# Optimization experiments

Measured on AMD Instinct MI355X. Metric: run time of the kernel, lower is better.

Reference implementation:

```python
import jax, jax.numpy as jnp
import numpy as np

B, C, H, W = 2048, 512, 4, 4
T, D, NH, HD, FF, NL = 16, 512, 8, 64, 1024, 4
EPS = 1e-5
SCALE = float(1.0 / np.sqrt(HD))


def _make_adj(h, w):
    # torch_geometric.utils.grid(h, w): 3x3 neighborhood incl. self-loop;
    # GCNConv sym-normalizes: A_hat = D^-1/2 A D^-1/2
    n = h * w
    A = np.zeros((n, n), np.float32)
    for r in range(h):
        for c in range(w):
            for dr in (-1, 0, 1):
                for dc in (-1, 0, 1):
                    rr, cc = r + dr, c + dc
                    if 0 <= rr < h and 0 <= cc < w:
                        A[r * w + c, rr * w + cc] = 1.0
    dinv = 1.0 / np.sqrt(A.sum(1))
    return (A * dinv[:, None] * dinv[None, :]).astype(np.float32)


def setup_inputs():
    key = jax.random.key(0)
    ks = iter(jax.random.split(key, 64))
    def w(*s):
        return jax.random.normal(next(ks), s, jnp.float32) * 0.02
    return dict(
        x=jax.random.normal(next(ks), (B, C, H, W), jnp.float32),
        emb_w=w(D, D), emb_b=jnp.zeros((D,), jnp.float32),
        emb_ln_g=jnp.ones((D,), jnp.float32), emb_ln_b=jnp.zeros((D,), jnp.float32),
        pos=w(1, T, D),
        attn_wq=w(NL, D, D), attn_wk=w(NL, D, D), attn_wv=w(NL, D, D),
        attn_bq=jnp.zeros((NL, D), jnp.float32), attn_bk=jnp.zeros((NL, D), jnp.float32),
        attn_bv=jnp.zeros((NL, D), jnp.float32),
        attn_wo=w(NL, D, D), attn_bo=jnp.zeros((NL, D), jnp.float32),
        ln1_g=jnp.ones((NL, D), jnp.float32), ln1_b=jnp.zeros((NL, D), jnp.float32),
        ff_w1=w(NL, D, FF), ff_b1=jnp.zeros((NL, FF), jnp.float32),
        ff_w2=w(NL, FF, D), ff_b2=jnp.zeros((NL, D), jnp.float32),
        ln2_g=jnp.ones((NL, D), jnp.float32), ln2_b=jnp.zeros((NL, D), jnp.float32),
        fc_w=w(D, D), fc_b=jnp.zeros((D,), jnp.float32),
        fc_ln_g=jnp.ones((D,), jnp.float32), fc_ln_b=jnp.zeros((D,), jnp.float32),
        gcn_w1=w(C, 2 * C), gcn_b1=jnp.zeros((2 * C,), jnp.float32),
        gcn_ln1_g=jnp.ones((2 * C,), jnp.float32), gcn_ln1_b=jnp.zeros((2 * C,), jnp.float32),
        gcn_w2=w(2 * C, C), gcn_b2=jnp.zeros((C,), jnp.float32),
        gcn_ln2_g=jnp.ones((C,), jnp.float32), gcn_ln2_b=jnp.zeros((C,), jnp.float32),
        fusion_w=w(C, 2 * C), fusion_b=jnp.zeros((C,), jnp.float32),
        adj=jnp.asarray(_make_adj(H, W)),
    )


def _ln(x, g, b):
    mu = x.mean(-1, keepdims=True)
    var = ((x - mu) ** 2).mean(-1, keepdims=True)
    return (x - mu) * jax.lax.rsqrt(var + EPS) * g + b


def reference(x, emb_w, emb_b, emb_ln_g, emb_ln_b, pos,
              attn_wq, attn_wk, attn_wv, attn_bq, attn_bk, attn_bv, attn_wo, attn_bo,
              ln1_g, ln1_b, ff_w1, ff_b1, ff_w2, ff_b2, ln2_g, ln2_b,
              fc_w, fc_b, fc_ln_g, fc_ln_b,
              gcn_w1, gcn_b1, gcn_ln1_g, gcn_ln1_b, gcn_w2, gcn_b2, gcn_ln2_g, gcn_ln2_b,
              fusion_w, fusion_b, adj):
    Bx = x.shape[0]
    # ---- transformer branch: tokens = 16 spatial positions, dim 512 ----
    h = x.reshape(Bx, C, T).transpose(0, 2, 1)                 # [B,T,D]
    h = _ln(h @ emb_w + emb_b, emb_ln_g, emb_ln_b) + pos
    for i in range(NL):  # post-norm TransformerEncoderLayer, ReLU, eval (no dropout)
        q = (h @ attn_wq[i] + attn_bq[i]).reshape(Bx, T, NH, HD).transpose(0, 2, 1, 3)
        k = (h @ attn_wk[i] + attn_bk[i]).reshape(Bx, T, NH, HD).transpose(0, 2, 1, 3)
        v = (h @ attn_wv[i] + attn_bv[i]).reshape(Bx, T, NH, HD).transpose(0, 2, 1, 3)
        a = jax.nn.softmax(jnp.einsum('bhqd,bhkd->bhqk', q, k) * SCALE, axis=-1)
        o = jnp.einsum('bhqk,bhkd->bhqd', a, v).transpose(0, 2, 1, 3).reshape(Bx, T, D)
        h = _ln(h + o @ attn_wo[i] + attn_bo[i], ln1_g[i], ln1_b[i])
        f = jax.nn.relu(h @ ff_w1[i] + ff_b1[i]) @ ff_w2[i] + ff_b2[i]
        h = _ln(h + f, ln2_g[i], ln2_b[i])
    h = _ln(h @ fc_w + fc_b, fc_ln_g, fc_ln_b)
    x1 = h.transpose(0, 2, 1).reshape(Bx, C, H, W)
    # ---- GCN branch: dense normalized adjacency over the 16-node grid ----
    xn = x.transpose(0, 2, 3, 1).reshape(Bx, T, C)             # [B,16,C]
    g = jnp.einsum('mn,bnd->bmd', adj, xn @ gcn_w1) + gcn_b1   # GCNConv1 (bias after aggr)
    g = jax.nn.elu(_ln(g, gcn_ln1_g, gcn_ln1_b))
    g = jnp.einsum('mn,bnd->bmd', adj, g @ gcn_w2) + gcn_b2    # GCNConv2
    g = jax.nn.elu(_ln(g, gcn_ln2_g, gcn_ln2_b))
    x2 = g.reshape(Bx, H, W, C).transpose(0, 3, 1, 2)
    # ---- fusion: 1x1 conv + InstanceNorm2d (no affine) + ELU ----
    xc = jnp.concatenate([x1, x2], axis=1)                     # [B,2C,H,W]
    y = jnp.einsum('oc,bchw->bohw', fusion_w, xc) + fusion_b[None, :, None, None]
    mu = y.mean((2, 3), keepdims=True)
    var = ((y - mu) ** 2).mean((2, 3), keepdims=True)
    y = (y - mu) * jax.lax.rsqrt(var + EPS)
    return jax.nn.elu(y)
```

## Files before the change

### kernel.cpp

```cpp
#include <hip/hip_runtime.h>


typedef _Float16 f16;
typedef f16 f16x8 __attribute__((ext_vector_type(8)));
typedef f16 f16x4 __attribute__((ext_vector_type(4)));
typedef float f32x4 __attribute__((ext_vector_type(4)));

__device__ inline float wred_sum(float s) {
#pragma unroll
  for (int m = 32; m; m >>= 1) s += __shfl_xor(s, m);
  return s;
}

struct WDesc {
  const float* src;
  f16* dst;
  int K, N, tiles_n, tile_base, mode;
};
struct WTable {
  WDesc d[32];
  int n;
};

__global__ void wconvert_kernel(WTable tab) {
  const int tile = blockIdx.x;
  int di = 0;
  while (di + 1 < tab.n && tab.d[di + 1].tile_base <= tile) ++di;
  const WDesc w = tab.d[di];
  const int t = tile - w.tile_base;
  const int tk = t / w.tiles_n, tn = t % w.tiles_n;
  const int tid = threadIdx.x;
  const int rr = tid >> 5, cc = tid & 31;
  __shared__ float tb[32][33];
  if (w.mode == 0) {
#pragma unroll
    for (int i = 0; i < 4; i++) {
      const int k = tk * 32 + i * 8 + rr, n = tn * 32 + cc;
      tb[i * 8 + rr][cc] = w.src[(size_t)k * w.N + n];
    }
    __syncthreads();
#pragma unroll
    for (int i = 0; i < 4; i++) {
      const int n = tn * 32 + i * 8 + rr, k = tk * 32 + cc;
      w.dst[(size_t)n * w.K + k] = (f16)tb[cc][i * 8 + rr];
    }
  } else {
#pragma unroll
    for (int i = 0; i < 4; i++) {
      const int k = tk * 32 + i * 8 + rr, n = tn * 32 + cc;
      w.dst[(size_t)k * w.N + n] = (f16)w.src[(size_t)k * w.N + n];
    }
  }
}

__global__ void biaspack_kernel(const float* __restrict__ bq,
                                const float* __restrict__ bk,
                                const float* __restrict__ bv,
                                float* __restrict__ bqkv) {
  const int i = blockIdx.x * 256 + threadIdx.x;
  if (i >= 4 * 1536) return;
  const int l = i / 1536, j = i % 1536;
  float v;
  if (j < 512)       v = bq[l * 512 + j];
  else if (j < 1024) v = bk[l * 512 + j - 512];
  else               v = bv[l * 512 + j - 1024];
  bqkv[i] = v;
}

__global__ void prep_kernel(const float* __restrict__ x, f16* __restrict__ X0) {
  const int b = blockIdx.x;
  for (int c = threadIdx.x; c < 512; c += 256) {
    const float* src = x + ((size_t)b * 512 + c) * 16;
    float vals[16];
#pragma unroll
    for (int i = 0; i < 4; i++) {
      const float4 v = ((const float4*)src)[i];
      vals[i * 4 + 0] = v.x; vals[i * 4 + 1] = v.y;
      vals[i * 4 + 2] = v.z; vals[i * 4 + 3] = v.w;
    }
#pragma unroll
    for (int t = 0; t < 16; t++)
      X0[((size_t)b * 16 + t) * 512 + c] = (f16)vals[t];
  }
}

template <int OUT, bool RELU, bool HASB>
__global__ __launch_bounds__(256) void gemm_kernel(
    const f16* __restrict__ A, const f16* __restrict__ Bt, void* __restrict__ C,
    const float* __restrict__ bias, int N, int K, int lda, int ldb) {
  __shared__ alignas(16) f16 sm[3][8192];
  const int tid = threadIdx.x;
  const int nb = N >> 7;
  const int cpx = gridDim.x >> 3;
  const int wg = (blockIdx.x & 7) * cpx + (blockIdx.x >> 3);
  const int bx = wg % nb;
  const int by = wg / nb;
  const int row0 = by << 7, col0 = bx << 7;
  const int lane = tid & 63;
  const int wave = tid >> 6;
  const int wm = (wave >> 1) << 6;
  const int wn = (wave & 1) << 6;
  const int srow = tid >> 2;
  const int schunk = (tid & 3) ^ ((tid >> 3) & 3);
  const f16* gA = A + (size_t)(row0 + srow) * lda + (schunk << 3);
  const f16* gB = Bt + (size_t)(col0 + srow) * ldb + (schunk << 3);
  const int wave_off = (tid & 0xC0) << 3;
  f32x4 acc[4][4] = {};
  const int rm = lane & 15;
  const int kg = lane >> 4;
  const int nt = K >> 5;

  auto STAGE = [&](int t, int bufi) {
    f16* lA = sm[bufi] + wave_off;
    f16* lB = sm[bufi] + 4096 + wave_off;
    const int kt = t << 5;
    __builtin_amdgcn_global_load_lds(
        (const __attribute__((address_space(1))) void*)(gA + kt),
        (__attribute__((address_space(3))) void*)lA, 16, 0, 0);
    __builtin_amdgcn_global_load_lds(
        (const __attribute__((address_space(1))) void*)(gA + (size_t)64 * lda + kt),
        (__attribute__((address_space(3))) void*)(lA + 2048), 16, 0, 0);
    __builtin_amdgcn_global_load_lds(
        (const __attribute__((address_space(1))) void*)(gB + kt),
        (__attribute__((address_space(3))) void*)lB, 16, 0, 0);
    __builtin_amdgcn_global_load_lds(
        (const __attribute__((address_space(1))) void*)(gB + (size_t)64 * ldb + kt),
        (__attribute__((address_space(3))) void*)(lB + 2048), 16, 0, 0);
  };

  STAGE(0, 0);
  STAGE(1, 1);
  asm volatile("s_waitcnt vmcnt(4)" ::: "memory");
  __builtin_amdgcn_s_barrier();

  for (int t = 0; t < nt; ++t) {
    const int cur = t % 3;
    if (t + 2 < nt) STAGE(t + 2, (t + 2) % 3);
    const f16* As = sm[cur];
    const f16* Bs = sm[cur] + 4096;
    f16x8 af[4], bf[4];
#pragma unroll
    for (int m = 0; m < 4; ++m) {
      const int r = wm + m * 16 + rm;
      af[m] = *(const f16x8*)(As + (r << 5) + ((kg ^ ((r >> 1) & 3)) << 3));
    }
#pragma unroll
    for (int n = 0; n < 4; ++n) {
      const int r = wn + n * 16 + rm;
      bf[n] = *(const f16x8*)(Bs + (r << 5) + ((kg ^ ((r >> 1) & 3)) << 3));
    }
#pragma unroll
    for (int m = 0; m < 4; ++m)
#pragma unroll
      for (int n = 0; n < 4; ++n)
        acc[m][n] =
            __builtin_amdgcn_mfma_f32_16x16x32_f16(af[m], bf[n], acc[m][n], 0, 0, 0);
    if (t + 2 < nt) {
      asm volatile("s_waitcnt vmcnt(4)" ::: "memory");
    } else {
      asm volatile("s_waitcnt vmcnt(0)" ::: "memory");
    }
    __builtin_amdgcn_s_barrier();
  }

  const int cn = lane & 15;
  const int rg = (lane >> 4) << 2;
  if (OUT == 3) {
    float* out = (float*)C;
#pragma unroll
    for (int m = 0; m < 4; ++m) {
      const int bidx = (row0 >> 4) + (wm >> 4) + m;
#pragma unroll
      for (int n = 0; n < 4; ++n) {
        const int col = col0 + wn + n * 16 + cn;
        const float v0 = acc[m][n][0], v1 = acc[m][n][1];
        const float v2 = acc[m][n][2], v3 = acc[m][n][3];
        float s = v0 + v1 + v2 + v3;
        s += __shfl_xor(s, 16);
        s += __shfl_xor(s, 32);
        const float mu = s * (1.f / 16.f);
        float q = (v0 - mu) * (v0 - mu) + (v1 - mu) * (v1 - mu) +
                  (v2 - mu) * (v2 - mu) + (v3 - mu) * (v3 - mu);
        q += __shfl_xor(q, 16);
        q += __shfl_xor(q, 32);
        const float rstd = rsqrtf(q * (1.f / 16.f) + 1e-5f);
        float4 z;
        z.x = (v0 - mu) * rstd; z.x = z.x > 0.f ? z.x : expm1f(z.x);
        z.y = (v1 - mu) * rstd; z.y = z.y > 0.f ? z.y : expm1f(z.y);
        z.z = (v2 - mu) * rstd; z.z = z.z > 0.f ? z.z : expm1f(z.z);
        z.w = (v3 - mu) * rstd; z.w = z.w > 0.f ? z.w : expm1f(z.w);
        *(float4*)(out + ((size_t)bidx * 512 + col) * 16 + rg) = z;
      }
    }
  } else {
#pragma unroll
    for (int m = 0; m < 4; ++m) {
#pragma unroll
      for (int n = 0; n < 4; ++n) {
        const int col = col0 + wn + n * 16 + cn;
        const float bv = HASB ? bias[col] : 0.0f;
#pragma unroll
        for (int r = 0; r < 4; ++r) {
          const int row = row0 + wm + m * 16 + rg + r;
          float v = acc[m][n][r] + bv;
          if (RELU) v = v > 0.f ? v : 0.f;
          ((f16*)C)[(size_t)row * N + col] = (f16)v;
        }
      }
    }
  }
}

template <bool RES, bool POS>
__global__ void ln_kernel(const f16* in, const f16* res, const float* g,
                          const float* b, const float* pos, f16* out) {
  const int row = (blockIdx.x << 2) + (threadIdx.x >> 6);
  const int lane = threadIdx.x & 63;
  const int c0 = lane << 3;
  float v[8];
  const f16x8 xi = *(const f16x8*)(in + (size_t)row * 512 + c0);
  if (RES) {
    const f16x8 ri = *(const f16x8*)(res + (size_t)row * 512 + c0);
#pragma unroll
    for (int j = 0; j < 8; j++) v[j] = (float)xi[j] + (float)ri[j];
  } else {
#pragma unroll
    for (int j = 0; j < 8; j++) v[j] = (float)xi[j];
  }
  float s = 0;
#pragma unroll
  for (int j = 0; j < 8; j++) s += v[j];
  s = wred_sum(s);
  const float mu = s * (1.f / 512.f);
  float q = 0;
#pragma unroll
  for (int j = 0; j < 8; j++) {
    const float d = v[j] - mu;
    q += d * d;
  }
  q = wred_sum(q);
  const float rstd = rsqrtf(q * (1.f / 512.f) + 1e-5f);
  const int t = row & 15;
  f16x8 o8;
#pragma unroll
  for (int j = 0; j < 8; j++) {
    float o = (v[j] - mu) * rstd * g[c0 + j] + b[c0 + j];
    if (POS) o += pos[t * 512 + c0 + j];
    o8[j] = (f16)o;
  }
  *(f16x8*)(out + (size_t)row * 512 + c0) = o8;
}

__global__ void lnpack_kernel(const f16* __restrict__ in, const f16* __restrict__ x2,
                              const float* __restrict__ g, const float* __restrict__ b,
                              f16* __restrict__ F) {
  const int row = (blockIdx.x << 2) + (threadIdx.x >> 6);
  const int lane = threadIdx.x & 63;
  const int c0 = lane << 3;
  const f16x8 xi = *(const f16x8*)(in + (size_t)row * 512 + c0);
  float v[8];
#pragma unroll
  for (int j = 0; j < 8; j++) v[j] = (float)xi[j];
  float s = 0;
#pragma unroll
  for (int j = 0; j < 8; j++) s += v[j];
  s = wred_sum(s);
  const float mu = s * (1.f / 512.f);
  float q = 0;
#pragma unroll
  for (int j = 0; j < 8; j++) {
    const float d = v[j] - mu;
    q += d * d;
  }
  q = wred_sum(q);
  const float rstd = rsqrtf(q * (1.f / 512.f) + 1e-5f);
  f16x8 o8;
#pragma unroll
  for (int j = 0; j < 8; j++)
    o8[j] = (f16)((v[j] - mu) * rstd * g[c0 + j] + b[c0 + j]);
  *(f16x8*)(F + (size_t)row * 1024 + c0) = o8;
  const f16x8 x2v = *(const f16x8*)(x2 + (size_t)row * 512 + c0);
  *(f16x8*)(F + (size_t)row * 1024 + 512 + c0) = x2v;
}

__global__ __launch_bounds__(256) void attn_kernel(const f16* __restrict__ qkv,
                                                   f16* __restrict__ o) {
  __shared__ f16 smem[4][3776];
  const int wid = threadIdx.x >> 6;
  const int lane = threadIdx.x & 63;
  const int bh = (blockIdx.x << 2) + wid;
  const int b = bh >> 3, h = bh & 7;
  f16* W = smem[wid];
  f16* Qw = W;
  f16* Kw = W + 1152;
  f16* Vw = W + 2304;
  f16* Pw = W + 3456;
  const size_t base = (size_t)b * 24576 + (size_t)h * 64;
#pragma unroll
  for (int i = 0; i < 6; i++) {
    const int c = i * 64 + lane;
    const int t = c / 24;
    const int rem = c - t * 24;
    const int mat = rem >> 3, ch = rem & 7;
    const f16x8 v = *(const f16x8*)(qkv + base + (size_t)t * 1536 + mat * 512 + ch * 8);
    *(f16x8*)(W + mat * 1152 + t * 72 + ch * 8) = v;
  }
  __syncthreads();
  const int rm = lane & 15, kg = lane >> 4;
  f32x4 s4 = {};
  {
    const f16x8 q0 = *(const f16x8*)(Qw + rm * 72 + kg * 8);
    const f16x8 q1 = *(const f16x8*)(Qw + rm * 72 + 32 + kg * 8);
    const f16x8 k0 = *(const f16x8*)(Kw + rm * 72 + kg * 8);
    const f16x8 k1 = *(const f16x8*)(Kw + rm * 72 + 32 + kg * 8);
    s4 = __builtin_amdgcn_mfma_f32_16x16x32_f16(q0, k0, s4, 0, 0, 0);
    s4 = __builtin_amdgcn_mfma_f32_16x16x32_f16(q1, k1, s4, 0, 0, 0);
  }
  float p[4];
#pragma unroll
  for (int r = 0; r < 4; r++) {
    const float sv = s4[r] * 0.125f;
    float m = sv;
    m = fmaxf(m, __shfl_xor(m, 1));
    m = fmaxf(m, __shfl_xor(m, 2));
    m = fmaxf(m, __shfl_xor(m, 4));
    m = fmaxf(m, __shfl_xor(m, 8));
    const float e = expf(sv - m);
    float s = e;
    s += __shfl_xor(s, 1);
    s += __shfl_xor(s, 2);
    s += __shfl_xor(s, 4);
    s += __shfl_xor(s, 8);
    p[r] = e / s;
  }
#pragma unroll
  for (int r = 0; r < 4; r++) Pw[(kg * 4 + r) * 20 + rm] = (f16)p[r];
  __syncthreads();
  const f16x4 pa = *(const f16x4*)(Pw + rm * 20 + kg * 4);
  f32x4 o4[4] = {};
#pragma unroll
  for (int dt = 0; dt < 4; dt++) {
    f16x4 vb;
#pragma unroll
    for (int kk = 0; kk < 4; kk++) vb[kk] = Vw[(kg * 4 + kk) * 72 + dt * 16 + rm];
    o4[dt] = __builtin_amdgcn_mfma_f32_16x16x16f16(pa, vb, o4[dt], 0, 0, 0);
  }
  f16* op = o + (size_t)b * 16 * 512 + (size_t)h * 64;
#pragma unroll
  for (int dt = 0; dt < 4; dt++)
#pragma unroll
    for (int r = 0; r < 4; r++)
      op[(size_t)(kg * 4 + r) * 512 + dt * 16 + rm] = (f16)o4[dt][r];
}

template <int DG>
__global__ __launch_bounds__(256) void adjmix_kernel(
    const f16* __restrict__ r, const float* __restrict__ adj,
    const float* __restrict__ bias, const float* __restrict__ g,
    const float* __restrict__ bet, f16* __restrict__ out, int ldo) {
  const int b = blockIdx.x;
  const int tid = threadIdx.x;
  __shared__ float agg[16][DG];
  __shared__ float adjs[256];
  if (tid < 256) adjs[tid] = adj[tid];
  __syncthreads();
  const int d0 = tid * 4;
  if (d0 < DG) {
    float acc[16][4];
#pragma unroll
    for (int m = 0; m < 16; m++)
#pragma unroll
      for (int j = 0; j < 4; j++) acc[m][j] = 0.f;
#pragma unroll
    for (int n = 0; n < 16; n++) {
      const f16x4 v = *(const f16x4*)(r + ((size_t)b * 16 + n) * DG + d0);
      const float v0 = (float)v[0], v1 = (float)v[1], v2 = (float)v[2], v3 = (float)v[3];
#pragma unroll
      for (int m = 0; m < 16; m++) {
        const float a = adjs[m * 16 + n];
        acc[m][0] += a * v0;
        acc[m][1] += a * v1;
        acc[m][2] += a * v2;
        acc[m][3] += a * v3;
      }
    }
    const float4 bv = *(const float4*)(bias + d0);
#pragma unroll
    for (int m = 0; m < 16; m++) {
      agg[m][d0 + 0] = acc[m][0] + bv.x;
      agg[m][d0 + 1] = acc[m][1] + bv.y;
      agg[m][d0 + 2] = acc[m][2] + bv.z;
      agg[m][d0 + 3] = acc[m][3] + bv.w;
    }
  }
  __syncthreads();
  const int wave = tid >> 6, lane = tid & 63;
  for (int m = wave; m < 16; m += 4) {
    float s = 0;
#pragma unroll
    for (int j = 0; j < DG / 64; j++) s += agg[m][j * 64 + lane];
    s = wred_sum(s);
    const float mu = s / DG;
    float q = 0;
#pragma unroll
    for (int j = 0; j < DG / 64; j++) {
      const float t = agg[m][j * 64 + lane] - mu;
      q += t * t;
    }
    q = wred_sum(q);
    const float rstd = rsqrtf(q / DG + 1e-5f);
    const size_t grow = (size_t)b * 16 + m;
#pragma unroll
    for (int j = 0; j < DG / 64; j++) {
      const int d = j * 64 + lane;
      float v = (agg[m][d] - mu) * rstd * g[d] + bet[d];
      v = v > 0.f ? v : expm1f(v);
      out[grow * ldo + d] = (f16)v;
    }
  }
}

extern "C" void kernel_launch(void* const* d_in, const int* in_sizes, int n_in,
                              void* d_out, int out_size, void* d_ws, size_t ws_size,
                              hipStream_t stream) {
  (void)in_sizes; (void)n_in; (void)out_size; (void)ws_size;
  const float* x         = (const float*)d_in[0];
  const float* emb_w     = (const float*)d_in[1];
  const float* emb_b     = (const float*)d_in[2];
  const float* emb_ln_g  = (const float*)d_in[3];
  const float* emb_ln_b  = (const float*)d_in[4];
  const float* pos       = (const float*)d_in[5];
  const float* attn_wq   = (const float*)d_in[6];
  const float* attn_wk   = (const float*)d_in[7];
  const float* attn_wv   = (const float*)d_in[8];
  const float* attn_bq   = (const float*)d_in[9];
  const float* attn_bk   = (const float*)d_in[10];
  const float* attn_bv   = (const float*)d_in[11];
  const float* attn_wo   = (const float*)d_in[12];
  const float* attn_bo   = (const float*)d_in[13];
  const float* ln1_g     = (const float*)d_in[14];
  const float* ln1_b     = (const float*)d_in[15];
  const float* ff_w1     = (const float*)d_in[16];
  const float* ff_b1     = (const float*)d_in[17];
  const float* ff_w2     = (const float*)d_in[18];
  const float* ff_b2     = (const float*)d_in[19];
  const float* ln2_g     = (const float*)d_in[20];
  const float* ln2_b     = (const float*)d_in[21];
  const float* fc_w      = (const float*)d_in[22];
  const float* fc_b      = (const float*)d_in[23];
  const float* fc_ln_g   = (const float*)d_in[24];
  const float* fc_ln_b   = (const float*)d_in[25];
  const float* gcn_w1    = (const float*)d_in[26];
  const float* gcn_b1    = (const float*)d_in[27];
  const float* gcn_ln1_g = (const float*)d_in[28];
  const float* gcn_ln1_b = (const float*)d_in[29];
  const float* gcn_w2    = (const float*)d_in[30];
  const float* gcn_b2    = (const float*)d_in[31];
  const float* gcn_ln2_g = (const float*)d_in[32];
  const float* gcn_ln2_b = (const float*)d_in[33];
  const float* fusion_w  = (const float*)d_in[34];
  const float* fusion_b  = (const float*)d_in[35];
  const float* adj       = (const float*)d_in[36];
  (void)fusion_b;

  char* ws = (char*)d_ws;
  f16*   WF   = (f16*)(ws);
  float* BQKV = (float*)(ws + 20971520ull);
  f16*   Ap   = (f16*)(ws + 20996096ull);
  f16*   Bp   = (f16*)(ws + 54550528ull);
  f16*   Cp   = (f16*)(ws + 88104960ull);
  f16*   Qp   = (f16*)(ws + 121659392ull);

  const size_t o_emb = 0, o_qkv = 262144, o_wo = 3407872, o_ff1 = 4456448,
               o_ff2 = 6553600, o_fc = 8650752, o_g1 = 8912896, o_g2 = 9437184,
               o_fus = 9961472;

  WTable tab{};
  int ntab = 0, tbase = 0;
  auto add = [&](const float* s, f16* dst, int K, int N, int mode) {
    WDesc& w = tab.d[ntab++];
    w.src = s; w.dst = dst; w.K = K; w.N = N;
    w.tiles_n = N / 32; w.tile_base = tbase; w.mode = mode;
    tbase += (K / 32) * (N / 32);
  };
  add(emb_w, WF + o_emb, 512, 512, 0);
  for (int l = 0; l < 4; l++) {
    add(attn_wq + l * 262144, WF + o_qkv + (size_t)l * 786432, 512, 512, 0);
    add(attn_wk + l * 262144, WF + o_qkv + (size_t)l * 786432 + 262144, 512, 512, 0);
    add(attn_wv + l * 262144, WF + o_qkv + (size_t)l * 786432 + 524288, 512, 512, 0);
  }
  for (int l = 0; l < 4; l++)
    add(attn_wo + l * 262144, WF + o_wo + (size_t)l * 262144, 512, 512, 0);
  for (int l = 0; l < 4; l++)
    add(ff_w1 + l * 524288, WF + o_ff1 + (size_t)l * 524288, 512, 1024, 0);
  for (int l = 0; l < 4; l++)
    add(ff_w2 + l * 524288, WF + o_ff2 + (size_t)l * 524288, 1024, 512, 0);
  add(fc_w, WF + o_fc, 512, 512, 0);
  add(gcn_w1, WF + o_g1, 512, 1024, 0);
  add(gcn_w2, WF + o_g2, 1024, 512, 0);
  add(fusion_w, WF + o_fus, 512, 1024, 1);
  tab.n = ntab;

  wconvert_kernel<<<tbase, 256, 0, stream>>>(tab);
  biaspack_kernel<<<24, 256, 0, stream>>>(attn_bq, attn_bk, attn_bv, BQKV);
  prep_kernel<<<2048, 256, 0, stream>>>(x, Ap);

  gemm_kernel<0, false, false><<<256 * 8, 256, 0, stream>>>(
      Ap, WF + o_g1, Qp, nullptr, 1024, 512, 512, 512);
  adjmix_kernel<1024><<<2048, 256, 0, stream>>>(
      Qp, adj, gcn_b1, gcn_ln1_g, gcn_ln1_b, Bp, 1024);
  gemm_kernel<0, false, false><<<256 * 4, 256, 0, stream>>>(
      Bp, WF + o_g2, Qp, nullptr, 512, 1024, 1024, 1024);

  gemm_kernel<0, false, true><<<256 * 4, 256, 0, stream>>>(
      Ap, WF + o_emb, Cp, emb_b, 512, 512, 512, 512);
  ln_kernel<false, true><<<8192, 256, 0, stream>>>(
      Cp, nullptr, emb_ln_g, emb_ln_b, pos, Bp);

  adjmix_kernel<512><<<2048, 256, 0, stream>>>(
      Qp, adj, gcn_b2, gcn_ln2_g, gcn_ln2_b, Ap, 512);

  for (int i = 0; i < 4; i++) {
    gemm_kernel<0, false, true><<<256 * 12, 256, 0, stream>>>(
        Bp, WF + o_qkv + (size_t)i * 786432, Qp, BQKV + i * 1536, 1536, 512, 512, 512);
    attn_kernel<<<4096, 256, 0, stream>>>(Qp, Cp);
    gemm_kernel<0, false, true><<<256 * 4, 256, 0, stream>>>(
        Cp, WF + o_wo + (size_t)i * 262144, Qp, attn_bo + i * 512, 512, 512, 512, 512);
    ln_kernel<true, false><<<8192, 256, 0, stream>>>(
        Qp, Bp, ln1_g + i * 512, ln1_b + i * 512, nullptr, Bp);
    gemm_kernel<0, true, true><<<256 * 8, 256, 0, stream>>>(
        Bp, WF + o_ff1 + (size_t)i * 524288, Qp, ff_b1 + i * 1024, 1024, 512, 512, 512);
    gemm_kernel<0, false, true><<<256 * 4, 256, 0, stream>>>(
        Qp, WF + o_ff2 + (size_t)i * 524288, Qp + 33554432ull, ff_b2 + i * 512,
        512, 1024, 1024, 1024);
    ln_kernel<true, false><<<8192, 256, 0, stream>>>(
        Qp + 33554432ull, Bp, ln2_g + i * 512, ln2_b + i * 512, nullptr, Bp);
  }

  gemm_kernel<0, false, true><<<256 * 4, 256, 0, stream>>>(
      Bp, WF + o_fc, Qp, fc_b, 512, 512, 512, 512);
  lnpack_kernel<<<8192, 256, 0, stream>>>(Qp, Ap, fc_ln_g, fc_ln_b, Bp);

  gemm_kernel<3, false, false><<<256 * 4, 256, 0, stream>>>(
      Bp, WF + o_fus, d_out, nullptr, 512, 1024, 1024, 1024);
}
```

Baseline: 1.335 ms.

## Switch GEMMs to 256x256 tiles with 512 threads and 4-stage LDS pipeline

Replaces the 128x128, 256-thread GEMM with a 256x256 tile kernel run by 8 waves. Each wave computes a 128x64 sub-tile, and K-loop staging deepens to 4 LDS buffers with a compile-time trip count. The larger tile is meant to raise operand reuse and cut global and LDS traffic per FLOP, while the deeper prefetch hides load latency. In exchange it uses 128KB of LDS and twice the accumulators, and grids shrink to a few hundred blocks, so only one block fits per CU and there is less latency hiding across blocks.

```diff
diff --git a/kernel.cpp b/kernel.cpp
--- a/kernel.cpp
+++ b/kernel.cpp
@@ -84,83 +84,84 @@
   }
 }
 
-template <int OUT, bool RELU, bool HASB>
-__global__ __launch_bounds__(256) void gemm_kernel(
+template <int OUT, bool RELU, bool HASB, int NT>
+__global__ __launch_bounds__(512) void gemm256_kernel(
     const f16* __restrict__ A, const f16* __restrict__ Bt, void* __restrict__ C,
-    const float* __restrict__ bias, int N, int K, int lda, int ldb) {
-  __shared__ alignas(16) f16 sm[3][8192];
+    const float* __restrict__ bias, int N, int lda, int ldb) {
+  __shared__ alignas(16) f16 sm[4][16384];
   const int tid = threadIdx.x;
-  const int nb = N >> 7;
+  const int nb = N >> 8;
   const int cpx = gridDim.x >> 3;
   const int wg = (blockIdx.x & 7) * cpx + (blockIdx.x >> 3);
-  const int bx = wg % nb;
-  const int by = wg / nb;
-  const int row0 = by << 7, col0 = bx << 7;
+  const int bx = wg % nb, by = wg / nb;
+  const int row0 = by << 8, col0 = bx << 8;
   const int lane = tid & 63;
-  const int wave = tid >> 6;
-  const int wm = (wave >> 1) << 6;
-  const int wn = (wave & 1) << 6;
+  const int wid = tid >> 6;
+  const int wm = (wid >> 2) << 7;
+  const int wn = (wid & 3) << 6;
   const int srow = tid >> 2;
-  const int schunk = (tid & 3) ^ ((tid >> 3) & 3);
+  const int schunk = (tid & 3) ^ (srow & 3);
   const f16* gA = A + (size_t)(row0 + srow) * lda + (schunk << 3);
   const f16* gB = Bt + (size_t)(col0 + srow) * ldb + (schunk << 3);
-  const int wave_off = (tid & 0xC0) << 3;
-  f32x4 acc[4][4] = {};
+  const unsigned ldsw = (unsigned)(tid & 0x1C0) << 3;
+  f32x4 acc[8][4] = {};
   const int rm = lane & 15;
   const int kg = lane >> 4;
-  const int nt = K >> 5;
-
-  auto STAGE = [&](int t, int bufi) {
-    f16* lA = sm[bufi] + wave_off;
-    f16* lB = sm[bufi] + 4096 + wave_off;
+  const int koff = (kg ^ (rm & 3)) << 3;
+
+  auto STAGE = [&](int t) {
+    f16* base = sm[t & 3];
     const int kt = t << 5;
     __builtin_amdgcn_global_load_lds(
         (const __attribute__((address_space(1))) void*)(gA + kt),
-        (__attribute__((address_space(3))) void*)lA, 16, 0, 0);
+        (__attribute__((address_space(3))) void*)(base + ldsw), 16, 0, 0);
     __builtin_amdgcn_global_load_lds(
-        (const __attribute__((address_space(1))) void*)(gA + (size_t)64 * lda + kt),
-        (__attribute__((address_space(3))) void*)(lA + 2048), 16, 0, 0);
+        (const __attribute__((address_space(1))) void*)(gA + (size_t)128 * lda + kt),
+        (__attribute__((address_space(3))) void*)(base + 4096 + ldsw), 16, 0, 0);
     __builtin_amdgcn_global_load_lds(
         (const __attribute__((address_space(1))) void*)(gB + kt),
-        (__attribute__((address_space(3))) void*)lB, 16, 0, 0);
+        (__attribute__((address_space(3))) void*)(base + 8192 + ldsw), 16, 0, 0);
     __builtin_amdgcn_global_load_lds(
-        (const __attribute__((address_space(1))) void*)(gB + (size_t)64 * ldb + kt),
-        (__attribute__((address_space(3))) void*)(lB + 2048), 16, 0, 0);
+        (const __attribute__((address_space(1))) void*)(gB + (size_t)128 * ldb + kt),
+        (__attribute__((address_space(3))) void*)(base + 12288 + ldsw), 16, 0, 0);
   };
 
-  STAGE(0, 0);
-  STAGE(1, 1);
-  asm volatile("s_waitcnt vmcnt(4)" ::: "memory");
+  STAGE(0);
+  STAGE(1);
+  STAGE(2);
+  asm volatile("s_waitcnt vmcnt(8)" ::: "memory");
   __builtin_amdgcn_s_barrier();
-
-  for (int t = 0; t < nt; ++t) {
-    const int cur = t % 3;
-    if (t + 2 < nt) STAGE(t + 2, (t + 2) % 3);
-    const f16* As = sm[cur];
-    const f16* Bs = sm[cur] + 4096;
-    f16x8 af[4], bf[4];
-#pragma unroll
-    for (int m = 0; m < 4; ++m) {
-      const int r = wm + m * 16 + rm;
-      af[m] = *(const f16x8*)(As + (r << 5) + ((kg ^ ((r >> 1) & 3)) << 3));
-    }
-#pragma unroll
-    for (int n = 0; n < 4; ++n) {
-      const int r = wn + n * 16 + rm;
-      bf[n] = *(const f16x8*)(Bs + (r << 5) + ((kg ^ ((r >> 1) & 3)) << 3));
-    }
-#pragma unroll
-    for (int m = 0; m < 4; ++m)
+  __builtin_amdgcn_sched_barrier(0);
+
+#pragma unroll 1
+  for (int t = 0; t < NT; ++t) {
+    if (t + 3 < NT) STAGE(t + 3);
+    const f16* As = sm[t & 3];
+    const f16* Bs = As + 8192;
+    f16x8 af[8], bf[4];
+#pragma unroll
+    for (int m = 0; m < 8; ++m)
+      af[m] = *(const f16x8*)(As + ((wm + m * 16 + rm) << 5) + koff);
+#pragma unroll
+    for (int n = 0; n < 4; ++n)
+      bf[n] = *(const f16x8*)(Bs + ((wn + n * 16 + rm) << 5) + koff);
+#pragma unroll
+    for (int m = 0; m < 8; ++m)
 #pragma unroll
       for (int n = 0; n < 4; ++n)
         acc[m][n] =
             __builtin_amdgcn_mfma_f32_16x16x32_f16(af[m], bf[n], acc[m][n], 0, 0, 0);
-    if (t + 2 < nt) {
+    if (t + 3 < NT) {
+      asm volatile("s_waitcnt vmcnt(8)" ::: "memory");
+    } else if (t + 2 < NT) {
       asm volatile("s_waitcnt vmcnt(4)" ::: "memory");
-    } else {
+    } else if (t + 1 < NT) {
       asm volatile("s_waitcnt vmcnt(0)" ::: "memory");
     }
-    __builtin_amdgcn_s_barrier();
+    if (t + 1 < NT) {
+      __builtin_amdgcn_s_barrier();
+      __builtin_amdgcn_sched_barrier(0);
+    }
   }
 
   const int cn = lane & 15;
@@ -168,7 +169,7 @@
   if (OUT == 3) {
     float* out = (float*)C;
 #pragma unroll
-    for (int m = 0; m < 4; ++m) {
+    for (int m = 0; m < 8; ++m) {
       const int bidx = (row0 >> 4) + (wm >> 4) + m;
 #pragma unroll
       for (int n = 0; n < 4; ++n) {
@@ -194,7 +195,7 @@
     }
   } else {
 #pragma unroll
-    for (int m = 0; m < 4; ++m) {
+    for (int m = 0; m < 8; ++m) {
 #pragma unroll
       for (int n = 0; n < 4; ++n) {
         const int col = col0 + wn + n * 16 + cn;
@@ -505,15 +506,15 @@
   biaspack_kernel<<<24, 256, 0, stream>>>(attn_bq, attn_bk, attn_bv, BQKV);
   prep_kernel<<<2048, 256, 0, stream>>>(x, Ap);
 
-  gemm_kernel<0, false, false><<<256 * 8, 256, 0, stream>>>(
-      Ap, WF + o_g1, Qp, nullptr, 1024, 512, 512, 512);
+  gemm256_kernel<0, false, false, 16><<<512, 512, 0, stream>>>(
+      Ap, WF + o_g1, Qp, nullptr, 1024, 512, 512);
   adjmix_kernel<1024><<<2048, 256, 0, stream>>>(
       Qp, adj, gcn_b1, gcn_ln1_g, gcn_ln1_b, Bp, 1024);
-  gemm_kernel<0, false, false><<<256 * 4, 256, 0, stream>>>(
-      Bp, WF + o_g2, Qp, nullptr, 512, 1024, 1024, 1024);
-
-  gemm_kernel<0, false, true><<<256 * 4, 256, 0, stream>>>(
-      Ap, WF + o_emb, Cp, emb_b, 512, 512, 512, 512);
+  gemm256_kernel<0, false, false, 32><<<256, 512, 0, stream>>>(
+      Bp, WF + o_g2, Qp, nullptr, 512, 1024, 1024);
+
+  gemm256_kernel<0, false, true, 16><<<256, 512, 0, stream>>>(
+      Ap, WF + o_emb, Cp, emb_b, 512, 512, 512);
   ln_kernel<false, true><<<8192, 256, 0, stream>>>(
       Cp, nullptr, emb_ln_g, emb_ln_b, pos, Bp);
 
@@ -521,26 +522,26 @@
       Qp, adj, gcn_b2, gcn_ln2_g, gcn_ln2_b, Ap, 512);
 
   for (int i = 0; i < 4; i++) {
-    gemm_kernel<0, false, true><<<256 * 12, 256, 0, stream>>>(
-        Bp, WF + o_qkv + (size_t)i * 786432, Qp, BQKV + i * 1536, 1536, 512, 512, 512);
+    gemm256_kernel<0, false, true, 16><<<768, 512, 0, stream>>>(
+        Bp, WF + o_qkv + (size_t)i * 786432, Qp, BQKV + i * 1536, 1536, 512, 512);
     attn_kernel<<<4096, 256, 0, stream>>>(Qp, Cp);
-    gemm_kernel<0, false, true><<<256 * 4, 256, 0, stream>>>(
-        Cp, WF + o_wo + (size_t)i * 262144, Qp, attn_bo + i * 512, 512, 512, 512, 512);
+    gemm256_kernel<0, false, true, 16><<<256, 512, 0, stream>>>(
+        Cp, WF + o_wo + (size_t)i * 262144, Qp, attn_bo + i * 512, 512, 512, 512);
     ln_kernel<true, false><<<8192, 256, 0, stream>>>(
         Qp, Bp, ln1_g + i * 512, ln1_b + i * 512, nullptr, Bp);
-    gemm_kernel<0, true, true><<<256 * 8, 256, 0, stream>>>(
-        Bp, WF + o_ff1 + (size_t)i * 524288, Qp, ff_b1 + i * 1024, 1024, 512, 512, 512);
-    gemm_kernel<0, false, true><<<256 * 4, 256, 0, stream>>>(
+    gemm256_kernel<0, true, true, 16><<<512, 512, 0, stream>>>(
+        Bp, WF + o_ff1 + (size_t)i * 524288, Qp, ff_b1 + i * 1024, 1024, 512, 512);
+    gemm256_kernel<0, false, true, 32><<<256, 512, 0, stream>>>(
         Qp, WF + o_ff2 + (size_t)i * 524288, Qp + 33554432ull, ff_b2 + i * 512,
-        512, 1024, 1024, 1024);
+        512, 1024, 1024);
     ln_kernel<true, false><<<8192, 256, 0, stream>>>(
         Qp + 33554432ull, Bp, ln2_g + i * 512, ln2_b + i * 512, nullptr, Bp);
   }
 
-  gemm_kernel<0, false, true><<<256 * 4, 256, 0, stream>>>(
-      Bp, WF + o_fc, Qp, fc_b, 512, 512, 512, 512);
+  gemm256_kernel<0, false, true, 16><<<256, 512, 0, stream>>>(
+      Bp, WF + o_fc, Qp, fc_b, 512, 512, 512);
   lnpack_kernel<<<8192, 256, 0, stream>>>(Qp, Ap, fc_ln_g, fc_ln_b, Bp);
 
-  gemm_kernel<3, false, false><<<256 * 4, 256, 0, stream>>>(
-      Bp, WF + o_fus, d_out, nullptr, 512, 1024, 1024, 1024);
-}
+  gemm256_kernel<3, false, false, 32><<<256, 512, 0, stream>>>(
+      Bp, WF + o_fus, d_out, nullptr, 512, 1024, 1024);
+}
```

After: 1.313 ms. No clear change (-1.6%).
